# Performance work log

Hardware: AMD Instinct MI355X
Metric: run time of the kernel (lower is better)

The kernel has to match this reference:

```python
import jax, jax.numpy as jnp
import numpy as np

B, L, D, DC, DH, H, DE, DO, DT = 4, 2048, 256, 256, 32, 8, 1024, 256, 256


def _ln(x, g, b, eps=1e-5):
    m = jnp.mean(x, -1, keepdims=True)
    v = jnp.mean((x - m) ** 2, -1, keepdims=True)
    return (x - m) * jax.lax.rsqrt(v + eps) * g + b


def setup_inputs() -> dict:
    key = jax.random.key(0)
    ks = jax.random.split(key, 16)

    def p(k, shape, s=0.02):
        return jax.random.normal(k, shape, jnp.float32) * s

    return dict(
        x=jax.random.normal(ks[0], (B, L, D), jnp.float32),
        context=jax.random.normal(ks[1], (B, L, DC), jnp.float32),
        t=jax.random.normal(ks[2], (B, DT), jnp.float32),
        pos_enc=jax.random.normal(ks[3], (1, L, D), jnp.float32),
        ln_g=jnp.ones(D), ln_b=jnp.zeros(D),
        Wq=p(ks[4], (D, DH * H)), bq=jnp.zeros(DH * H),
        Wkv1=p(ks[5], (DC, DC)), bkv1=jnp.zeros(DC),
        kvln_g=jnp.ones(DC), kvln_b=jnp.zeros(DC),
        Wkv2=p(ks[6], (DC, (DH + D) * H)), bkv2=jnp.zeros((DH + D) * H),
        Wm=p(ks[7], (D * H, D)), bm=jnp.zeros(D),
        Wt1=p(ks[8], (DT, DT)), bt1=jnp.zeros(DT),
        Wt2=p(ks[9], (DT, D + DE)), bt2=jnp.zeros(D + DE),
        ff1ln_g=jnp.ones(D), ff1ln_b=jnp.zeros(D),
        Wff1=p(ks[10], (D, DE)), bff1=jnp.zeros(DE),
        Wff2=p(ks[11], (DE, DO)), bff2=jnp.zeros(DO),
    )


def reference(x, context, t, pos_enc, ln_g, ln_b, Wq, bq, Wkv1, bkv1,
              kvln_g, kvln_b, Wkv2, bkv2, Wm, bm, Wt1, bt1, Wt2, bt2,
              ff1ln_g, ff1ln_b, Wff1, bff1, Wff2, bff2):
    silu = jax.nn.silu
    # q_proj = Swish -> Linear, applied to ln(x) + pos_enc
    q = silu(_ln(x, ln_g, ln_b) + pos_enc) @ Wq + bq          # [B,L,H*DH]
    q = q.reshape(B, L, H, DH)
    # kv_proj = Linear -> LayerNorm -> Swish -> Linear
    kv = silu(_ln(context @ Wkv1 + bkv1, kvln_g, kvln_b)) @ Wkv2 + bkv2
    k = kv[..., : DH * H].reshape(B, L, H, DH)
    v = kv[..., DH * H:].reshape(B, L, H, D)                   # v head dim = d_in
    scale = DH ** -0.5
    attn = jnp.einsum('bnhc,bmhc->bhnm', q, k) * scale         # [B,H,L,L]
    # mask = 1 - triu(ones): True strictly BELOW the diagonal (anti-causal)
    mask = jnp.tril(jnp.ones((L, L), bool), -1)
    attn = jnp.where(mask, -jnp.inf, attn)
    attn = jax.nn.softmax(attn, axis=-1)
    out = jnp.einsum('bhnm,bmhc->bnhc', attn, v).reshape(B, L, H * D)
    x = x + out @ Wm + bm
    # FiLM time conditioning: [B, d_in+d_expand] -> [B, 1, ...]
    th = silu(t @ Wt1 + bt1) @ Wt2 + bt2
    t_shift = th[:, None, :D]
    t_scale = th[:, None, D:]
    h = silu(_ln(x + t_shift, ff1ln_g, ff1ln_b)) @ Wff1 + bff1
    # ff2 = Swish -> Dropout(eval) -> Linear; shortcut is Identity (d_in == d_out)
    return silu(h * jax.nn.sigmoid(t_scale)) @ Wff2 + bff2 + x
```

## Files before the change

kernel.cpp:

```cpp
#include <hip/hip_runtime.h>
#include <hip/hip_bf16.h>

#define DEVI __device__ __forceinline__
using u16 = unsigned short;
using u32 = unsigned int;

typedef __attribute__((ext_vector_type(4))) float f32x4;
typedef __attribute__((ext_vector_type(8))) __bf16 bf16x8;

constexpr int L_ = 2048;

DEVI u16 f2bf(float f){
  u32 u = __builtin_bit_cast(u32, f);
  u32 r = u + 0x7FFFu + ((u >> 16) & 1u);
  return (u16)(r >> 16);
}
DEVI float sigm(float x){ return 1.f / (1.f + __expf(-x)); }

DEVI f32x4 mfma16(bf16x8 a, bf16x8 b, f32x4 c){
  return __builtin_amdgcn_mfma_f32_16x16x32_bf16(a, b, c, 0, 0, 0);
}

DEVI void gload16(const u16* src, u16* lds){
  __builtin_amdgcn_global_load_lds(
      (const __attribute__((address_space(1))) u32*)src,
      (__attribute__((address_space(3))) u32*)lds, 16, 0, 0);
}
DEVI void gload4(const u16* src, u16* lds){
  __builtin_amdgcn_global_load_lds(
      (const __attribute__((address_space(1))) u32*)src,
      (__attribute__((address_space(3))) u32*)lds, 4, 0, 0);
}

#define WAITV(N) asm volatile("s_waitcnt vmcnt(" #N ")" ::: "memory")

__global__ __launch_bounds__(256)
void prep_all(const float* __restrict__ Wq,   u16* __restrict__ wtq,
              const float* __restrict__ Wkv1, u16* __restrict__ wtkv1,
              const float* __restrict__ Wkv2, u16* __restrict__ wtkv2,
              const float* __restrict__ Wm,   u16* __restrict__ wtm,
              const float* __restrict__ Wff1, u16* __restrict__ wtff1,
              const float* __restrict__ Wff2, u16* __restrict__ wtff2,
              const float* __restrict__ tvec, const float* __restrict__ Wt1,
              const float* __restrict__ bt1,  float* __restrict__ ub,
              const float* __restrict__ ctx,  u16* __restrict__ ctx_bf,
              const float* __restrict__ x,    const float* __restrict__ pos,
              const float* __restrict__ ln_g, const float* __restrict__ ln_b,
              u16* __restrict__ qin_bf){
  __shared__ float smem[32 * 33];
  const int id = blockIdx.x;
  if (id >= 3780){
    const int row  = (id - 3780) * 4 + (threadIdx.x >> 6);
    const int lane = threadIdx.x & 63;
    const long base = (long)row * 256 + lane * 4;
    float4 x4 = *(const float4*)(x + base);
    float v[4] = {x4.x, x4.y, x4.z, x4.w};
    float s = v[0] + v[1] + v[2] + v[3];
    #pragma unroll
    for (int d = 1; d < 64; d <<= 1) s += __shfl_xor(s, d);
    const float mean = s * (1.f / 256.f);
    float q = 0.f;
    #pragma unroll
    for (int i = 0; i < 4; ++i){ float dd = v[i] - mean; q += dd * dd; }
    #pragma unroll
    for (int d = 1; d < 64; d <<= 1) q += __shfl_xor(q, d);
    const float rstd = rsqrtf(q * (1.f / 256.f) + 1e-5f);
    float4 g4 = *(const float4*)(ln_g + lane * 4);
    float4 b4 = *(const float4*)(ln_b + lane * 4);
    float4 pp = *(const float4*)(pos + (long)(row & (L_ - 1)) * 256 + lane * 4);
    float gv[4] = {g4.x, g4.y, g4.z, g4.w}, bb[4] = {b4.x, b4.y, b4.z, b4.w};
    float pe[4] = {pp.x, pp.y, pp.z, pp.w};
    ushort4 o; u16 tmp[4];
    #pragma unroll
    for (int i = 0; i < 4; ++i){
      float y = (v[i] - mean) * rstd * gv[i] + bb[i] + pe[i];
      y = y * sigm(y);
      tmp[i] = f2bf(y);
    }
    o.x = tmp[0]; o.y = tmp[1]; o.z = tmp[2]; o.w = tmp[3];
    *(ushort4*)(qin_bf + base) = o;
    return;
  }
  if (id >= 1732){
    long i = ((long)(id - 1732) * 256 + threadIdx.x) * 4;
    float4 v = *(const float4*)(ctx + i);
    ushort4 o; o.x = f2bf(v.x); o.y = f2bf(v.y); o.z = f2bf(v.z); o.w = f2bf(v.w);
    *(ushort4*)(ctx_bf + i) = o;
    return;
  }
  if (id >= 1728){
    int b = id - 1728, j = threadIdx.x;
    smem[j] = tvec[b * 256 + j];
    __syncthreads();
    float acc = bt1[j];
    for (int k = 0; k < 256; ++k) acc += smem[k] * Wt1[k * 256 + j];
    ub[b * 256 + j] = acc * sigm(acc);
    return;
  }
  const float* W; u16* WT; int K, N, local, nx;
  if      (id <   64){ W = Wq;   WT = wtq;   K = 256;  N = 256;  local = id;        nx = 8;  }
  else if (id <  128){ W = Wkv1; WT = wtkv1; K = 256;  N = 256;  local = id - 64;   nx = 8;  }
  else if (id <  704){ W = Wkv2; WT = wtkv2; K = 256;  N = 2304; local = id - 128;  nx = 72; }
  else if (id < 1216){ W = Wm;   WT = wtm;   K = 2048; N = 256;  local = id - 704;  nx = 8;  }
  else if (id < 1472){ W = Wff1; WT = wtff1; K = 256;  N = 1024; local = id - 1216; nx = 32; }
  else               { W = Wff2; WT = wtff2; K = 1024; N = 256;  local = id - 1472; nx = 8;  }
  int n0 = (local % nx) * 32, k0 = (local / nx) * 32;
  float (*tile)[33] = (float(*)[33])smem;
  int tx = threadIdx.x & 31, ty = threadIdx.x >> 5;
  #pragma unroll
  for (int i = 0; i < 4; ++i){ int kk = ty + i*8; tile[kk][tx] = W[(long)(k0+kk)*N + n0 + tx]; }
  __syncthreads();
  #pragma unroll
  for (int i = 0; i < 4; ++i){ int nn = ty + i*8; WT[(long)(n0+nn)*K + k0 + tx] = f2bf(tile[tx][nn]); }
}

template<int MODE>
__global__ __launch_bounds__(256)
void ln_silu(const float* __restrict__ in, const float* __restrict__ add,
             const float* __restrict__ g, const float* __restrict__ bvec,
             u16* __restrict__ out){
  const int row  = blockIdx.x * 4 + (threadIdx.x >> 6);
  const int lane = threadIdx.x & 63;
  const long base = (long)row * 256 + lane * 4;
  float4 x4 = *(const float4*)(in + base);
  float v[4] = {x4.x, x4.y, x4.z, x4.w};
  if constexpr (MODE == 2){
    float4 s4 = *(const float4*)(add + (row >> 11) * 1280 + lane * 4);
    v[0] += s4.x; v[1] += s4.y; v[2] += s4.z; v[3] += s4.w;
  }
  float s = v[0] + v[1] + v[2] + v[3];
  #pragma unroll
  for (int d = 1; d < 64; d <<= 1) s += __shfl_xor(s, d);
  const float mean = s * (1.f / 256.f);
  float q = 0.f;
  #pragma unroll
  for (int i = 0; i < 4; ++i){ float dd = v[i] - mean; q += dd * dd; }
  #pragma unroll
  for (int d = 1; d < 64; d <<= 1) q += __shfl_xor(q, d);
  const float rstd = rsqrtf(q * (1.f / 256.f) + 1e-5f);
  float4 g4 = *(const float4*)(g + lane * 4);
  float4 b4 = *(const float4*)(bvec + lane * 4);
  float gv[4] = {g4.x, g4.y, g4.z, g4.w}, bb[4] = {b4.x, b4.y, b4.z, b4.w};
  ushort4 o; u16 tmp[4];
  #pragma unroll
  for (int i = 0; i < 4; ++i){
    float y = (v[i] - mean) * rstd * gv[i] + bb[i];
    y = y * sigm(y);
    tmp[i] = f2bf(y);
  }
  o.x = tmp[0]; o.y = tmp[1]; o.z = tmp[2]; o.w = tmp[3];
  *(ushort4*)(out + base) = o;
}

template<int EPI>
DEVI void gemm_body(const u16* __restrict__ A, const u16* __restrict__ BT,
                    const float* __restrict__ bias, const float* __restrict__ res,
                    const float* __restrict__ thv,
                    float* __restrict__ outF, u16* __restrict__ outB, u16* __restrict__ outB2,
                    int N, int K, u16* smem, int by){
  u16* As = smem;
  u16* Bs = smem + 3 * 4096;
  const int t = threadIdx.x, lane = t & 63;
  const int lr = lane & 15, lg = lane >> 4;
  const int wv = t >> 6;
  const int wrow = (wv >> 2) * 32;
  const int wcol = (wv & 3) * 32;
  const long bm = (long)blockIdx.x * 64, bn = (long)by * 128;

  auto stage = [&](int step, int buf){
    const int kt = step * 64;
    {
      int o = t * 16;
      int row = o >> 7, cb = o & 127;
      int scb = cb ^ ((row & 7) << 4);
      gload16(&A[(bm + row) * K + kt + (scb >> 1)], &As[buf * 4096 + (o >> 1)]);
    }
    #pragma unroll
    for (int i = 0; i < 2; ++i){
      int o = t * 16 + i * 8192;
      int row = o >> 7, cb = o & 127;
      int scb = cb ^ ((row & 7) << 4);
      gload16(&BT[(bn + row) * K + kt + (scb >> 1)], &Bs[buf * 8192 + (o >> 1)]);
    }
  };

  const f32x4 zero = {0.f, 0.f, 0.f, 0.f};
  f32x4 acc[2][2];
  acc[0][0] = zero; acc[0][1] = zero; acc[1][0] = zero; acc[1][1] = zero;

  const int ns = K >> 6;
  stage(0, 0); stage(1, 1);
  int bufc = 0;
  for (int i = 0; i < ns; ++i){
    if (i + 1 < ns) WAITV(3); else WAITV(0);
    __builtin_amdgcn_s_barrier();
    __builtin_amdgcn_sched_barrier(0);
    if (i + 2 < ns){
      int nb = bufc + 2; if (nb >= 3) nb -= 3;
      stage(i + 2, nb);
    }
    __builtin_amdgcn_s_setprio(1);
    #pragma unroll
    for (int ks = 0; ks < 2; ++ks){
      bf16x8 av[2], bv[2];
      const int cb = (ks * 32 + lg * 8) * 2;
      #pragma unroll
      for (int m = 0; m < 2; ++m){
        int row = wrow + m * 16 + lr;
        av[m] = *(const bf16x8*)((const char*)&As[bufc * 4096] + row * 128 + (cb ^ ((row & 7) << 4)));
      }
      #pragma unroll
      for (int n = 0; n < 2; ++n){
        int row = wcol + n * 16 + lr;
        bv[n] = *(const bf16x8*)((const char*)&Bs[bufc * 8192] + row * 128 + (cb ^ ((row & 7) << 4)));
      }
      #pragma unroll
      for (int m = 0; m < 2; ++m)
        #pragma unroll
        for (int n = 0; n < 2; ++n)
          acc[m][n] = mfma16(av[m], bv[n], acc[m][n]);
    }
    __builtin_amdgcn_s_setprio(0);
    bufc = (bufc + 1 == 3) ? 0 : bufc + 1;
  }

  constexpr float QSC = 0.17677669529663687f * 1.4426950408889634f;

  if constexpr (EPI == 3){
    if (by >= 2){
      __syncthreads();
      u16* tile = smem;
      #pragma unroll
      for (int m = 0; m < 2; ++m)
        #pragma unroll
        for (int n = 0; n < 2; ++n){
          int c_l = wcol + n * 16 + lr;
          long col = bn + c_l;
          int rbase = wrow + m * 16 + lg * 4;
          ushort4 pk;
          u16* pp = (u16*)&pk;
          #pragma unroll
          for (int r = 0; r < 4; ++r)
            pp[r] = f2bf(acc[m][n][r] + bias[col]);
          *(ushort4*)&tile[c_l * 72 + rbase] = pk;
        }
      __syncthreads();
      const int b = (int)(bm >> 11), l0 = (int)(bm & 2047);
      const int hdb = (int)bn - 256;
      const int h = hdb >> 8, d0 = hdb & 255;
      const int dd = t >> 2, lh = (t & 3) * 16;
      u16* dst = outB2 + ((long)((b * 8 + h) * 256 + d0 + dd)) * 2048 + l0 + lh;
      *(uint4*)(dst + 0) = *(const uint4*)&tile[dd * 72 + lh + 0];
      *(uint4*)(dst + 8) = *(const uint4*)&tile[dd * 72 + lh + 8];
      return;
    }
    #pragma unroll
    for (int m = 0; m < 2; ++m)
      #pragma unroll
      for (int n = 0; n < 2; ++n)
        #pragma unroll
        for (int r = 0; r < 4; ++r){
          long row = bm + wrow + m * 16 + lg * 4 + r;
          long col = bn + wcol + n * 16 + lr;
          outB[row * 256 + col] = f2bf(acc[m][n][r] + bias[col]);
        }
    return;
  }

  #pragma unroll
  for (int m = 0; m < 2; ++m)
    #pragma unroll
    for (int n = 0; n < 2; ++n)
      #pragma unroll
      for (int r = 0; r < 4; ++r){
        long row = bm + wrow + m * 16 + lg * 4 + r;
        long col = bn + wcol + n * 16 + lr;
        float v = acc[m][n][r] + bias[col];
        if constexpr (EPI == 0){
          outB[row * N + col] = f2bf(v);
        } else if constexpr (EPI == 1){
          outF[row * N + col] = v;
        } else if constexpr (EPI == 2){
          outF[row * N + col] = v + res[row * N + col];
        } else if constexpr (EPI == 4){
          int b = (int)(row >> 11);
          float ts = thv[b * 1280 + 256 + (int)col];
          float z = v * sigm(ts);
          outB[row * N + col] = f2bf(z * sigm(z));
        } else {
          outB[row * N + col] = f2bf(v * QSC);
        }
      }
}

template<int EPI>
__global__ __launch_bounds__(512, 4)
void gemm2(const u16* __restrict__ A, const u16* __restrict__ BT,
           const float* __restrict__ bias, const float* __restrict__ res,
           const float* __restrict__ thv,
           float* __restrict__ outF, u16* __restrict__ outB, u16* __restrict__ outB2,
           int M, int N, int K){
  __shared__ u16 smem[3 * 4096 + 3 * 8192];
  gemm_body<EPI>(A, BT, bias, res, thv, outF, outB, outB2, N, K, smem, blockIdx.y);
}

template<int E0, int E1>
__global__ __launch_bounds__(512, 4)
void gemm2_dual(const u16* __restrict__ A0, const u16* __restrict__ B0,
                const float* __restrict__ bias0, u16* __restrict__ out0,
                const u16* __restrict__ A1, const u16* __restrict__ B1,
                const float* __restrict__ bias1, float* __restrict__ out1,
                const float* __restrict__ ub, const float* __restrict__ Wt2,
                const float* __restrict__ bt2, float* __restrict__ th,
                int N, int K){
  __shared__ u16 smem[3 * 4096 + 3 * 8192];
  if (blockIdx.y == 4){
    if (blockIdx.x >= 20) return;
    float* us = (float*)smem;
    int local = blockIdx.x, b = local & 3, jb = local >> 2;
    int tj = threadIdx.x & 255;
    us[tj] = ub[b * 256 + tj];
    __syncthreads();
    int j = jb * 256 + tj;
    float acc = bt2[j];
    for (int k = 0; k < 256; ++k) acc += us[k] * Wt2[k * 1280 + j];
    th[b * 1280 + j] = acc;
    return;
  }
  if (blockIdx.y < 2)
    gemm_body<E0>(A0, B0, bias0, nullptr, nullptr, nullptr, out0, nullptr, N, K, smem, blockIdx.y);
  else
    gemm_body<E1>(A1, B1, bias1, nullptr, nullptr, out1, nullptr, nullptr, N, K, smem, blockIdx.y - 2);
}

__global__ __launch_bounds__(256, 2)
void gemm3(const u16* __restrict__ A, const u16* __restrict__ BT,
           const float* __restrict__ bias, const float* __restrict__ res,
           float* __restrict__ outF, int M, int N, int K){
  __shared__ u16 smem[3 * 2048 + 3 * 8192];
  u16* As = smem;
  u16* Bs = smem + 3 * 2048;
  const int t = threadIdx.x, lane = t & 63;
  const int lr = lane & 15, lg = lane >> 4;
  const int wcol = (t >> 6) * 32;
  const long bm = (long)blockIdx.x * 32, bn = (long)blockIdx.y * 128;

  auto stage = [&](int step, int buf){
    const int kt = step * 64;
    {
      int o = t * 16;
      int row = o >> 7, cb = o & 127;
      int scb = cb ^ ((row & 7) << 4);
      gload16(&A[(bm + row) * K + kt + (scb >> 1)], &As[buf * 2048 + (o >> 1)]);
    }
    #pragma unroll
    for (int i = 0; i < 4; ++i){
      int o = t * 16 + i * 4096;
      int row = o >> 7, cb = o & 127;
      int scb = cb ^ ((row & 7) << 4);
      gload16(&BT[(bn + row) * K + kt + (scb >> 1)], &Bs[buf * 8192 + (o >> 1)]);
    }
  };

  const f32x4 zero = {0.f, 0.f, 0.f, 0.f};
  f32x4 acc[2][2];
  acc[0][0] = zero; acc[0][1] = zero; acc[1][0] = zero; acc[1][1] = zero;

  const int ns = K >> 6;
  stage(0, 0); stage(1, 1);
  int bufc = 0;
  for (int i = 0; i < ns; ++i){
    if (i + 1 < ns) WAITV(5); else WAITV(0);
    __builtin_amdgcn_s_barrier();
    __builtin_amdgcn_sched_barrier(0);
    if (i + 2 < ns){
      int nb = bufc + 2; if (nb >= 3) nb -= 3;
      stage(i + 2, nb);
    }
    __builtin_amdgcn_s_setprio(1);
    #pragma unroll
    for (int ks = 0; ks < 2; ++ks){
      bf16x8 av[2], bv[2];
      const int cb = (ks * 32 + lg * 8) * 2;
      #pragma unroll
      for (int m = 0; m < 2; ++m){
        int row = m * 16 + lr;
        av[m] = *(const bf16x8*)((const char*)&As[bufc * 2048] + row * 128 + (cb ^ ((row & 7) << 4)));
      }
      #pragma unroll
      for (int n = 0; n < 2; ++n){
        int row = wcol + n * 16 + lr;
        bv[n] = *(const bf16x8*)((const char*)&Bs[bufc * 8192] + row * 128 + (cb ^ ((row & 7) << 4)));
      }
      #pragma unroll
      for (int m = 0; m < 2; ++m)
        #pragma unroll
        for (int n = 0; n < 2; ++n)
          acc[m][n] = mfma16(av[m], bv[n], acc[m][n]);
    }
    __builtin_amdgcn_s_setprio(0);
    bufc = (bufc + 1 == 3) ? 0 : bufc + 1;
  }

  #pragma unroll
  for (int m = 0; m < 2; ++m)
    #pragma unroll
    for (int n = 0; n < 2; ++n)
      #pragma unroll
      for (int r = 0; r < 4; ++r){
        long row = bm + m * 16 + lg * 4 + r;
        long col = bn + wcol + n * 16 + lr;
        float v = acc[m][n][r] + bias[col];
        outF[row * N + col] = v + res[row * N + col];
      }
}

__global__ __launch_bounds__(512, 2)
void attn7(const u16* __restrict__ Q, const u16* __restrict__ Kb,
           const u16* __restrict__ VT, u16* __restrict__ attout){
  const int bh = blockIdx.x, b = bh >> 3, h = bh & 7;
  const int p  = blockIdx.y;
  const int t  = threadIdx.x;
  const int w  = t >> 6, lane = t & 63, lr = lane & 15, lg = lane >> 4;

  __shared__ u16 Vs[3][256 * 64];
  __shared__ u16 Ks[3][64 * 32];
  __shared__ u16 Ps[8][16 * 64];
  u16* myP = &Ps[w][0];

  const f32x4 zero = {0.f, 0.f, 0.f, 0.f};
  const u16* vbase = VT + (long)bh * 256 * 2048;
  const u16* kbase = Kb + (long)(b * L_) * 256 + h * 32;

  auto stage = [&](int m0, int buf){
    #pragma unroll
    for (int i = 0; i < 4; ++i){
      int ob = t * 16 + i * 8192;
      int d = ob >> 7, cb = ob & 127;
      int scb = cb ^ ((d & 7) << 4);
      gload16(vbase + (long)d * 2048 + m0 + (scb >> 1), &Vs[buf][ob >> 1]);
    }
    #pragma unroll
    for (int i = 0; i < 2; ++i){
      int g = t + i * 512;
      int row = g >> 4, sl = g & 15;
      int scol = ((sl & 3) << 1) + ((((sl >> 2) ^ (row & 3))) << 3);
      gload4(kbase + (long)(m0 + row) * 256 + scol, &Ks[buf][g << 1]);
    }
  };

  for (int half = 0; half < 2; ++half){
    const int chunk = half ? (15 - p) : p;
    const int n0 = chunk * 128;
    const int n_lo = n0 + w * 16;
    const int nt = (L_ - n0) >> 6;

    bf16x8 qf = *(const bf16x8*)(Q + ((long)(b * L_ + n_lo + lr)) * 256 + h * 32 + lg * 8);

    f32x4 o[16];
    #pragma unroll
    for (int c2 = 0; c2 < 16; ++c2) o[c2] = zero;
    float mrun = -1e30f, srun = 0.f;

    stage(n0, 0); stage(n0 + 64, 1);

    int bufc = 0;
    for (int tt = 0; tt < nt; ++tt){
      const int m0 = n0 + tt * 64;
      if (tt + 1 < nt) WAITV(6); else WAITV(0);
      __builtin_amdgcn_s_barrier();
      __builtin_amdgcn_sched_barrier(0);
      if (tt + 2 < nt){
        int nb = bufc + 2; if (nb >= 3) nb -= 3;
        stage(m0 + 128, nb);
      }

      if (m0 + 64 > n_lo){
        const bool partial = (m0 < n_lo + 16);

        bf16x8 kf[4];
        #pragma unroll
        for (int c = 0; c < 4; ++c){
          int row = c * 16 + lr;
          kf[c] = *(const bf16x8*)&Ks[bufc][row * 32 + ((lg ^ (row & 3)) << 3)];
        }
        f32x4 sc[4];
        #pragma unroll
        for (int c = 0; c < 4; ++c)
          sc[c] = mfma16(kf[c], qf, zero);

        if (partial){
          #pragma unroll
          for (int c = 0; c < 4; ++c)
            #pragma unroll
            for (int r = 0; r < 4; ++r)
              if ((m0 + c * 16 + lg * 4 + r) < (n_lo + lr)) sc[c][r] = -1e30f;
        }

        float t0 = fmaxf(fmaxf(sc[0][0], sc[0][1]), fmaxf(sc[0][2], sc[0][3]));
        #pragma unroll
        for (int c = 1; c < 4; ++c)
          t0 = fmaxf(t0, fmaxf(fmaxf(sc[c][0], sc[c][1]), fmaxf(sc[c][2], sc[c][3])));
        t0 = fmaxf(t0, __shfl_xor(t0, 16));
        t0 = fmaxf(t0, __shfl_xor(t0, 32));
        const bool needl = (t0 > mrun + 11.5f);
        if (__any(needl)){
          float mn  = fmaxf(mrun, t0);
          float frc = exp2f(mrun - mn);
          mrun = mn; srun *= frc;
          float f0 = __shfl(frc, lg * 4 + 0), f1 = __shfl(frc, lg * 4 + 1);
          float f2 = __shfl(frc, lg * 4 + 2), f3 = __shfl(frc, lg * 4 + 3);
          f32x4 fv = {f0, f1, f2, f3};
          #pragma unroll
          for (int c2 = 0; c2 < 16; ++c2) o[c2] *= fv;
        }

        {
          const int q = lr, sw = (q & 7) << 3;
          float rs = 0.f;
          #pragma unroll
          for (int c = 0; c < 4; ++c){
            float e0 = exp2f(sc[c][0] - mrun);
            float e1 = exp2f(sc[c][1] - mrun);
            float e2 = exp2f(sc[c][2] - mrun);
            float e3 = exp2f(sc[c][3] - mrun);
            if (partial && mrun < -1e29f){ e0 = e1 = e2 = e3 = 0.f; }
            rs += (e0 + e1) + (e2 + e3);
            ushort4 pk;
            pk.x = __builtin_bit_cast(u16, (__bf16)e0);
            pk.y = __builtin_bit_cast(u16, (__bf16)e1);
            pk.z = __builtin_bit_cast(u16, (__bf16)e2);
            pk.w = __builtin_bit_cast(u16, (__bf16)e3);
            *(ushort4*)&myP[q * 64 + ((c * 16 + lg * 4) ^ sw)] = pk;
          }
          rs += __shfl_xor(rs, 16);
          rs += __shfl_xor(rs, 32);
          srun += rs;
        }

        __builtin_amdgcn_s_setprio(1);
        #pragma unroll
        for (int ks = 0; ks < 2; ++ks){
          bf16x8 pa = *(const bf16x8*)&myP[lr * 64 + ((ks * 32 + lg * 8) ^ ((lr & 7) << 3))];
          #pragma unroll
          for (int c2 = 0; c2 < 16; ++c2){
            const int d = c2 * 16 + lr;
            bf16x8 vf = *(const bf16x8*)((const char*)&Vs[bufc][0] + d * 128 +
                                         ((ks * 64 + lg * 16) ^ ((d & 7) << 4)));
            o[c2] = mfma16(pa, vf, o[c2]);
          }
        }
        __builtin_amdgcn_s_setprio(0);
      }
      bufc = (bufc + 1 == 3) ? 0 : bufc + 1;
    }

    {
      float invc = 1.f / srun;
      #pragma unroll
      for (int r = 0; r < 4; ++r){
        float inv = __shfl(invc, lg * 4 + r);
        long row = (long)(b * L_ + n_lo + lg * 4 + r);
        #pragma unroll
        for (int c2 = 0; c2 < 16; ++c2)
          attout[row * 2048 + h * 256 + c2 * 16 + lr] = f2bf(o[c2][r] * inv);
      }
    }
    WAITV(0);
    __syncthreads();
  }
}

extern "C" void kernel_launch(void* const* d_in, const int* in_sizes, int n_in,
                              void* d_out, int out_size, void* d_ws, size_t ws_size,
                              hipStream_t stream){
  (void)in_sizes; (void)n_in; (void)out_size; (void)ws_size;
  const float* x    = (const float*)d_in[0];
  const float* ctx  = (const float*)d_in[1];
  const float* tin  = (const float*)d_in[2];
  const float* pos  = (const float*)d_in[3];
  const float* ln_g = (const float*)d_in[4];
  const float* ln_b = (const float*)d_in[5];
  const float* Wq   = (const float*)d_in[6];
  const float* bq   = (const float*)d_in[7];
  const float* Wkv1 = (const float*)d_in[8];
  const float* bkv1 = (const float*)d_in[9];
  const float* kvg  = (const float*)d_in[10];
  const float* kvb  = (const float*)d_in[11];
  const float* Wkv2 = (const float*)d_in[12];
  const float* bkv2 = (const float*)d_in[13];
  const float* Wm   = (const float*)d_in[14];
  const float* bm   = (const float*)d_in[15];
  const float* Wt1  = (const float*)d_in[16];
  const float* bt1  = (const float*)d_in[17];
  const float* Wt2  = (const float*)d_in[18];
  const float* bt2  = (const float*)d_in[19];
  const float* fg   = (const float*)d_in[20];
  const float* fb   = (const float*)d_in[21];
  const float* Wff1 = (const float*)d_in[22];
  const float* bff1 = (const float*)d_in[23];
  const float* Wff2 = (const float*)d_in[24];
  const float* bff2 = (const float*)d_in[25];

  char* ws = (char*)d_ws;
  u16*   wt_q   = (u16*)  (ws + 0);
  u16*   wt_kv1 = (u16*)  (ws + 131072);
  u16*   wt_kv2 = (u16*)  (ws + 262144);
  u16*   wt_m   = (u16*)  (ws + 1441792);
  u16*   wt_ff1 = (u16*)  (ws + 2490368);
  u16*   wt_ff2 = (u16*)  (ws + 3014656);
  u16*   ctx_bf = (u16*)  (ws + 3538944);
  u16*   qin_bf = (u16*)  (ws + 7733248);
  u16*   q_bf   = (u16*)  (ws + 11927552);
  float* kv1    = (float*)(ws + 16121856);
  u16*   k_bf   = (u16*)  (ws + 24510464);
  u16*   v_bf   = (u16*)  (ws + 28704768);
  u16*   vT     = (u16*)  (ws + 62259200);
  float* ub     = (float*)(ws + 95813632);
  float* th     = (float*)(ws + 95817728);

  prep_all<<<5828, 256, 0, stream>>>(Wq, wt_q, Wkv1, wt_kv1, Wkv2, wt_kv2,
                                     Wm, wt_m, Wff1, wt_ff1, Wff2, wt_ff2,
                                     tin, Wt1, bt1, ub,
                                     ctx, ctx_bf, x, pos, ln_g, ln_b, qin_bf);
  gemm2_dual<5,1><<<dim3(128, 5), 512, 0, stream>>>(qin_bf, wt_q, bq, q_bf,
                                                    ctx_bf, wt_kv1, bkv1, kv1,
                                                    ub, Wt2, bt2, th,
                                                    256, 256);
  ln_silu<1><<<2048, 256, 0, stream>>>(kv1, nullptr, kvg, kvb, qin_bf);
  gemm2<3><<<dim3(128, 18), 512, 0, stream>>>(qin_bf, wt_kv2, bkv2, nullptr, nullptr,
                                              nullptr, k_bf, vT, 8192, 2304, 256);
  attn7<<<dim3(32, 8), 512, 0, stream>>>(q_bf, k_bf, vT, v_bf);
  gemm3<<<dim3(256, 2), 256, 0, stream>>>(v_bf, wt_m, bm, x, kv1, 8192, 256, 2048);
  ln_silu<2><<<2048, 256, 0, stream>>>(kv1, th, fg, fb, ctx_bf);
  gemm2<4><<<dim3(128, 8), 512, 0, stream>>>(ctx_bf, wt_ff1, bff1, nullptr, th,
                                             nullptr, (u16*)vT, nullptr, 8192, 1024, 256);
  gemm3<<<dim3(256, 2), 256, 0, stream>>>((u16*)vT, wt_ff2, bff2, kv1,
                                          (float*)d_out, 8192, 256, 1024);
}
```

Measured before the change: 183.5 us.

## Restructure attention: 4 waves with 32 query rows each, K in registers

The attention kernel moves from 8 waves of 16 query rows, each block handling two paired chunks, to 4 waves of 32 query rows, with one chunk per block over a grid twice as large. Each V fragment read from shared memory now feeds two MFMAs, which halves LDS traffic per unit of compute. K tiles are loaded straight into registers with a prefetch one step ahead instead of being staged through LDS, and V triple buffering becomes double buffering. In exchange it doubles the output accumulator registers, which may raise spilling or lower occupancy, and loses some load-balance pairing within a block.

```diff
diff --git a/kernel.cpp b/kernel.cpp
--- a/kernel.cpp
+++ b/kernel.cpp
@@ -25,11 +25,6 @@
   __builtin_amdgcn_global_load_lds(
       (const __attribute__((address_space(1))) u32*)src,
       (__attribute__((address_space(3))) u32*)lds, 16, 0, 0);
-}
-DEVI void gload4(const u16* src, u16* lds){
-  __builtin_amdgcn_global_load_lds(
-      (const __attribute__((address_space(1))) u32*)src,
-      (__attribute__((address_space(3))) u32*)lds, 4, 0, 0);
 }
 
 #define WAITV(N) asm volatile("s_waitcnt vmcnt(" #N ")" ::: "memory")
@@ -415,159 +410,178 @@
       }
 }
 
-__global__ __launch_bounds__(512, 2)
-void attn7(const u16* __restrict__ Q, const u16* __restrict__ Kb,
-           const u16* __restrict__ VT, u16* __restrict__ attout){
+__global__ __launch_bounds__(256, 2)
+void attn11(const u16* __restrict__ Q, const u16* __restrict__ Kb,
+            const u16* __restrict__ VT, u16* __restrict__ attout){
   const int bh = blockIdx.x, b = bh >> 3, h = bh & 7;
-  const int p  = blockIdx.y;
-  const int t  = threadIdx.x;
-  const int w  = t >> 6, lane = t & 63, lr = lane & 15, lg = lane >> 4;
-
-  __shared__ u16 Vs[3][256 * 64];
-  __shared__ u16 Ks[3][64 * 32];
-  __shared__ u16 Ps[8][16 * 64];
+  const int yc = blockIdx.y;
+  const int chunk = (yc < 8) ? yc : 23 - yc;
+  const int n0 = chunk * 128;
+  const int t = threadIdx.x;
+  const int w = t >> 6, lane = t & 63, lr = lane & 15, lg = lane >> 4;
+  const int n_lo = n0 + w * 32;
+  const int nt = (L_ - n0) >> 6;
+
+  __shared__ u16 Vs[2][256 * 64];
+  __shared__ u16 Ps[4][32 * 64];
   u16* myP = &Ps[w][0];
 
   const f32x4 zero = {0.f, 0.f, 0.f, 0.f};
   const u16* vbase = VT + (long)bh * 256 * 2048;
   const u16* kbase = Kb + (long)(b * L_) * 256 + h * 32;
 
-  auto stage = [&](int m0, int buf){
-    #pragma unroll
-    for (int i = 0; i < 4; ++i){
-      int ob = t * 16 + i * 8192;
+  auto stageV = [&](int m0, int buf){
+    #pragma unroll
+    for (int i = 0; i < 8; ++i){
+      int ob = t * 16 + i * 4096;
       int d = ob >> 7, cb = ob & 127;
       int scb = cb ^ ((d & 7) << 4);
       gload16(vbase + (long)d * 2048 + m0 + (scb >> 1), &Vs[buf][ob >> 1]);
     }
-    #pragma unroll
-    for (int i = 0; i < 2; ++i){
-      int g = t + i * 512;
-      int row = g >> 4, sl = g & 15;
-      int scol = ((sl & 3) << 1) + ((((sl >> 2) ^ (row & 3))) << 3);
-      gload4(kbase + (long)(m0 + row) * 256 + scol, &Ks[buf][g << 1]);
-    }
   };
 
-  for (int half = 0; half < 2; ++half){
-    const int chunk = half ? (15 - p) : p;
-    const int n0 = chunk * 128;
-    const int n_lo = n0 + w * 16;
-    const int nt = (L_ - n0) >> 6;
-
-    bf16x8 qf = *(const bf16x8*)(Q + ((long)(b * L_ + n_lo + lr)) * 256 + h * 32 + lg * 8);
-
-    f32x4 o[16];
-    #pragma unroll
-    for (int c2 = 0; c2 < 16; ++c2) o[c2] = zero;
-    float mrun = -1e30f, srun = 0.f;
-
-    stage(n0, 0); stage(n0 + 64, 1);
-
-    int bufc = 0;
-    for (int tt = 0; tt < nt; ++tt){
-      const int m0 = n0 + tt * 64;
-      if (tt + 1 < nt) WAITV(6); else WAITV(0);
-      __builtin_amdgcn_s_barrier();
-      __builtin_amdgcn_sched_barrier(0);
-      if (tt + 2 < nt){
-        int nb = bufc + 2; if (nb >= 3) nb -= 3;
-        stage(m0 + 128, nb);
-      }
-
-      if (m0 + 64 > n_lo){
-        const bool partial = (m0 < n_lo + 16);
-
-        bf16x8 kf[4];
-        #pragma unroll
-        for (int c = 0; c < 4; ++c){
-          int row = c * 16 + lr;
-          kf[c] = *(const bf16x8*)&Ks[bufc][row * 32 + ((lg ^ (row & 3)) << 3)];
-        }
-        f32x4 sc[4];
+  bf16x8 qf[2];
+  #pragma unroll
+  for (int qh = 0; qh < 2; ++qh)
+    qf[qh] = *(const bf16x8*)(Q + ((long)(b * L_ + n_lo + qh * 16 + lr)) * 256 + h * 32 + lg * 8);
+
+  f32x4 o[2][16];
+  #pragma unroll
+  for (int qh = 0; qh < 2; ++qh)
+    #pragma unroll
+    for (int c2 = 0; c2 < 16; ++c2) o[qh][c2] = zero;
+  float mrun[2] = {-1e30f, -1e30f}, srun[2] = {0.f, 0.f};
+
+  stageV(n0, 0);
+  bf16x8 kf[4];
+  #pragma unroll
+  for (int c = 0; c < 4; ++c)
+    kf[c] = *(const bf16x8*)(kbase + (long)(n0 + c * 16 + lr) * 256 + lg * 8);
+
+  for (int tt = 0; tt < nt; ++tt){
+    const int m0 = n0 + tt * 64;
+    const int cur = tt & 1;
+    if (tt + 1 < nt) WAITV(4); else WAITV(0);
+    __builtin_amdgcn_s_barrier();
+    __builtin_amdgcn_sched_barrier(0);
+    bf16x8 kfN[4];
+    if (tt + 1 < nt){
+      stageV(m0 + 64, cur ^ 1);
+      #pragma unroll
+      for (int c = 0; c < 4; ++c)
+        kfN[c] = *(const bf16x8*)(kbase + (long)(m0 + 64 + c * 16 + lr) * 256 + lg * 8);
+    }
+
+    if (m0 + 64 > n_lo){
+      const bool partial = (m0 < n_lo + 32);
+
+      f32x4 sc[2][4];
+      #pragma unroll
+      for (int qh = 0; qh < 2; ++qh)
         #pragma unroll
         for (int c = 0; c < 4; ++c)
-          sc[c] = mfma16(kf[c], qf, zero);
-
-        if (partial){
+          sc[qh][c] = mfma16(kf[c], qf[qh], zero);
+
+      if (partial){
+        #pragma unroll
+        for (int qh = 0; qh < 2; ++qh)
           #pragma unroll
           for (int c = 0; c < 4; ++c)
             #pragma unroll
             for (int r = 0; r < 4; ++r)
-              if ((m0 + c * 16 + lg * 4 + r) < (n_lo + lr)) sc[c][r] = -1e30f;
-        }
-
-        float t0 = fmaxf(fmaxf(sc[0][0], sc[0][1]), fmaxf(sc[0][2], sc[0][3]));
+              if ((m0 + c * 16 + lg * 4 + r) < (n_lo + qh * 16 + lr)) sc[qh][c][r] = -1e30f;
+      }
+
+      float tmax[2]; bool needl = false;
+      #pragma unroll
+      for (int qh = 0; qh < 2; ++qh){
+        float t0 = fmaxf(fmaxf(sc[qh][0][0], sc[qh][0][1]), fmaxf(sc[qh][0][2], sc[qh][0][3]));
         #pragma unroll
         for (int c = 1; c < 4; ++c)
-          t0 = fmaxf(t0, fmaxf(fmaxf(sc[c][0], sc[c][1]), fmaxf(sc[c][2], sc[c][3])));
+          t0 = fmaxf(t0, fmaxf(fmaxf(sc[qh][c][0], sc[qh][c][1]),
+                               fmaxf(sc[qh][c][2], sc[qh][c][3])));
         t0 = fmaxf(t0, __shfl_xor(t0, 16));
         t0 = fmaxf(t0, __shfl_xor(t0, 32));
-        const bool needl = (t0 > mrun + 11.5f);
-        if (__any(needl)){
-          float mn  = fmaxf(mrun, t0);
-          float frc = exp2f(mrun - mn);
-          mrun = mn; srun *= frc;
+        tmax[qh] = t0;
+        needl |= (t0 > mrun[qh] + 11.5f);
+      }
+      if (__any(needl)){
+        #pragma unroll
+        for (int qh = 0; qh < 2; ++qh){
+          float mn  = fmaxf(mrun[qh], tmax[qh]);
+          float frc = exp2f(mrun[qh] - mn);
+          mrun[qh] = mn; srun[qh] *= frc;
           float f0 = __shfl(frc, lg * 4 + 0), f1 = __shfl(frc, lg * 4 + 1);
           float f2 = __shfl(frc, lg * 4 + 2), f3 = __shfl(frc, lg * 4 + 3);
           f32x4 fv = {f0, f1, f2, f3};
           #pragma unroll
-          for (int c2 = 0; c2 < 16; ++c2) o[c2] *= fv;
+          for (int c2 = 0; c2 < 16; ++c2) o[qh][c2] *= fv;
         }
-
-        {
-          const int q = lr, sw = (q & 7) << 3;
-          float rs = 0.f;
+      }
+
+      #pragma unroll
+      for (int qh = 0; qh < 2; ++qh){
+        const int q = qh * 16 + lr;
+        const int sw = (q & 7) << 3;
+        float rs = 0.f;
+        #pragma unroll
+        for (int c = 0; c < 4; ++c){
+          float e0 = exp2f(sc[qh][c][0] - mrun[qh]);
+          float e1 = exp2f(sc[qh][c][1] - mrun[qh]);
+          float e2 = exp2f(sc[qh][c][2] - mrun[qh]);
+          float e3 = exp2f(sc[qh][c][3] - mrun[qh]);
+          if (partial && mrun[qh] < -1e29f){ e0 = e1 = e2 = e3 = 0.f; }
+          rs += (e0 + e1) + (e2 + e3);
+          ushort4 pk;
+          pk.x = __builtin_bit_cast(u16, (__bf16)e0);
+          pk.y = __builtin_bit_cast(u16, (__bf16)e1);
+          pk.z = __builtin_bit_cast(u16, (__bf16)e2);
+          pk.w = __builtin_bit_cast(u16, (__bf16)e3);
+          *(ushort4*)&myP[q * 64 + ((c * 16 + lg * 4) ^ sw)] = pk;
+        }
+        rs += __shfl_xor(rs, 16);
+        rs += __shfl_xor(rs, 32);
+        srun[qh] += rs;
+      }
+
+      __builtin_amdgcn_s_setprio(1);
+      #pragma unroll
+      for (int ks = 0; ks < 2; ++ks){
+        bf16x8 pa[2];
+        #pragma unroll
+        for (int qh = 0; qh < 2; ++qh){
+          const int q = qh * 16 + lr;
+          pa[qh] = *(const bf16x8*)&myP[q * 64 + ((ks * 32 + lg * 8) ^ ((q & 7) << 3))];
+        }
+        #pragma unroll
+        for (int c2 = 0; c2 < 16; ++c2){
+          const int d = c2 * 16 + lr;
+          bf16x8 vf = *(const bf16x8*)((const char*)&Vs[cur][0] + d * 128 +
+                                       ((ks * 64 + lg * 16) ^ ((d & 7) << 4)));
           #pragma unroll
-          for (int c = 0; c < 4; ++c){
-            float e0 = exp2f(sc[c][0] - mrun);
-            float e1 = exp2f(sc[c][1] - mrun);
-            float e2 = exp2f(sc[c][2] - mrun);
-            float e3 = exp2f(sc[c][3] - mrun);
-            if (partial && mrun < -1e29f){ e0 = e1 = e2 = e3 = 0.f; }
-            rs += (e0 + e1) + (e2 + e3);
-            ushort4 pk;
-            pk.x = __builtin_bit_cast(u16, (__bf16)e0);
-            pk.y = __builtin_bit_cast(u16, (__bf16)e1);
-            pk.z = __builtin_bit_cast(u16, (__bf16)e2);
-            pk.w = __builtin_bit_cast(u16, (__bf16)e3);
-            *(ushort4*)&myP[q * 64 + ((c * 16 + lg * 4) ^ sw)] = pk;
-          }
-          rs += __shfl_xor(rs, 16);
-          rs += __shfl_xor(rs, 32);
-          srun += rs;
+          for (int qh = 0; qh < 2; ++qh)
+            o[qh][c2] = mfma16(pa[qh], vf, o[qh][c2]);
         }
-
-        __builtin_amdgcn_s_setprio(1);
-        #pragma unroll
-        for (int ks = 0; ks < 2; ++ks){
-          bf16x8 pa = *(const bf16x8*)&myP[lr * 64 + ((ks * 32 + lg * 8) ^ ((lr & 7) << 3))];
-          #pragma unroll
-          for (int c2 = 0; c2 < 16; ++c2){
-            const int d = c2 * 16 + lr;
-            bf16x8 vf = *(const bf16x8*)((const char*)&Vs[bufc][0] + d * 128 +
-                                         ((ks * 64 + lg * 16) ^ ((d & 7) << 4)));
-            o[c2] = mfma16(pa, vf, o[c2]);
-          }
-        }
-        __builtin_amdgcn_s_setprio(0);
-      }
-      bufc = (bufc + 1 == 3) ? 0 : bufc + 1;
-    }
-
-    {
-      float invc = 1.f / srun;
-      #pragma unroll
-      for (int r = 0; r < 4; ++r){
-        float inv = __shfl(invc, lg * 4 + r);
-        long row = (long)(b * L_ + n_lo + lg * 4 + r);
-        #pragma unroll
-        for (int c2 = 0; c2 < 16; ++c2)
-          attout[row * 2048 + h * 256 + c2 * 16 + lr] = f2bf(o[c2][r] * inv);
-      }
-    }
-    WAITV(0);
-    __syncthreads();
+      }
+      __builtin_amdgcn_s_setprio(0);
+    }
+    if (tt + 1 < nt){
+      #pragma unroll
+      for (int c = 0; c < 4; ++c) kf[c] = kfN[c];
+    }
+  }
+
+  #pragma unroll
+  for (int qh = 0; qh < 2; ++qh){
+    float invc = 1.f / srun[qh];
+    #pragma unroll
+    for (int r = 0; r < 4; ++r){
+      float inv = __shfl(invc, lg * 4 + r);
+      long row = (long)(b * L_ + n_lo + qh * 16 + lg * 4 + r);
+      #pragma unroll
+      for (int c2 = 0; c2 < 16; ++c2)
+        attout[row * 2048 + h * 256 + c2 * 16 + lr] = f2bf(o[qh][c2][r] * inv);
+    }
   }
 }
 
@@ -630,7 +644,7 @@
   ln_silu<1><<<2048, 256, 0, stream>>>(kv1, nullptr, kvg, kvb, qin_bf);
   gemm2<3><<<dim3(128, 18), 512, 0, stream>>>(qin_bf, wt_kv2, bkv2, nullptr, nullptr,
                                               nullptr, k_bf, vT, 8192, 2304, 256);
-  attn7<<<dim3(32, 8), 512, 0, stream>>>(q_bf, k_bf, vT, v_bf);
+  attn11<<<dim3(32, 16), 256, 0, stream>>>(q_bf, k_bf, vT, v_bf);
   gemm3<<<dim3(256, 2), 256, 0, stream>>>(v_bf, wt_m, bm, x, kv1, 8192, 256, 2048);
   ln_silu<2><<<2048, 256, 0, stream>>>(kv1, th, fg, fb, ctx_bf);
   gemm2<4><<<dim3(128, 8), 512, 0, stream>>>(ctx_bf, wt_ff1, bff1, nullptr, th,
```

New measurement: 219.2 us. 19.5% more time.

## Restructure attention pipeline into paired 128-key steps with direct K register loads

Applied to the files above, without the earlier changes.

The attention kernel now stages V tiles in pairs of 64-key buffers, one 128-key step at a time, with double buffering (4 buffers). A barrier and full vmcnt wait happen once per 128 keys instead of once per 64. K is no longer staged through LDS with 4-byte async loads; each wave reads its K fragments straight from global memory into registers. This is meant to cut barrier and wait overhead and drop the small K LDS copies. In exchange, per-wave global K loads are uncoalesced and sit on the critical path, and the full vmcnt(0) wait reduces overlap between loads and compute.

```diff
diff --git a/kernel.cpp b/kernel.cpp
--- a/kernel.cpp
+++ b/kernel.cpp
@@ -25,11 +25,6 @@
   __builtin_amdgcn_global_load_lds(
       (const __attribute__((address_space(1))) u32*)src,
       (__attribute__((address_space(3))) u32*)lds, 16, 0, 0);
-}
-DEVI void gload4(const u16* src, u16* lds){
-  __builtin_amdgcn_global_load_lds(
-      (const __attribute__((address_space(1))) u32*)src,
-      (__attribute__((address_space(3))) u32*)lds, 4, 0, 0);
 }
 
 #define WAITV(N) asm volatile("s_waitcnt vmcnt(" #N ")" ::: "memory")
@@ -416,15 +411,14 @@
 }
 
 __global__ __launch_bounds__(512, 2)
-void attn7(const u16* __restrict__ Q, const u16* __restrict__ Kb,
-           const u16* __restrict__ VT, u16* __restrict__ attout){
+void attn13(const u16* __restrict__ Q, const u16* __restrict__ Kb,
+            const u16* __restrict__ VT, u16* __restrict__ attout){
   const int bh = blockIdx.x, b = bh >> 3, h = bh & 7;
   const int p  = blockIdx.y;
   const int t  = threadIdx.x;
   const int w  = t >> 6, lane = t & 63, lr = lane & 15, lg = lane >> 4;
 
-  __shared__ u16 Vs[3][256 * 64];
-  __shared__ u16 Ks[3][64 * 32];
+  __shared__ u16 Vs[4][256 * 64];
   __shared__ u16 Ps[8][16 * 64];
   u16* myP = &Ps[w][0];
 
@@ -432,7 +426,7 @@
   const u16* vbase = VT + (long)bh * 256 * 2048;
   const u16* kbase = Kb + (long)(b * L_) * 256 + h * 32;
 
-  auto stage = [&](int m0, int buf){
+  auto stageV = [&](int m0, int buf){
     #pragma unroll
     for (int i = 0; i < 4; ++i){
       int ob = t * 16 + i * 8192;
@@ -440,20 +434,13 @@
       int scb = cb ^ ((d & 7) << 4);
       gload16(vbase + (long)d * 2048 + m0 + (scb >> 1), &Vs[buf][ob >> 1]);
     }
-    #pragma unroll
-    for (int i = 0; i < 2; ++i){
-      int g = t + i * 512;
-      int row = g >> 4, sl = g & 15;
-      int scol = ((sl & 3) << 1) + ((((sl >> 2) ^ (row & 3))) << 3);
-      gload4(kbase + (long)(m0 + row) * 256 + scol, &Ks[buf][g << 1]);
-    }
   };
 
   for (int half = 0; half < 2; ++half){
     const int chunk = half ? (15 - p) : p;
     const int n0 = chunk * 128;
     const int n_lo = n0 + w * 16;
-    const int nt = (L_ - n0) >> 6;
+    const int ntp = (L_ - n0) >> 7;
 
     bf16x8 qf = *(const bf16x8*)(Q + ((long)(b * L_ + n_lo + lr)) * 256 + h * 32 + lg * 8);
 
@@ -462,97 +449,99 @@
     for (int c2 = 0; c2 < 16; ++c2) o[c2] = zero;
     float mrun = -1e30f, srun = 0.f;
 
-    stage(n0, 0); stage(n0 + 64, 1);
-
-    int bufc = 0;
-    for (int tt = 0; tt < nt; ++tt){
-      const int m0 = n0 + tt * 64;
-      if (tt + 1 < nt) WAITV(6); else WAITV(0);
+    stageV(n0, 0); stageV(n0 + 64, 1);
+
+    auto tilec = [&](const bf16x8* kf, int m0, int buf){
+      if (m0 + 64 <= n_lo) return;
+      const bool partial = (m0 < n_lo + 16);
+
+      f32x4 sc[4];
+      #pragma unroll
+      for (int c = 0; c < 4; ++c)
+        sc[c] = mfma16(kf[c], qf, zero);
+
+      if (partial){
+        #pragma unroll
+        for (int c = 0; c < 4; ++c)
+          #pragma unroll
+          for (int r = 0; r < 4; ++r)
+            if ((m0 + c * 16 + lg * 4 + r) < (n_lo + lr)) sc[c][r] = -1e30f;
+      }
+
+      float t0 = fmaxf(fmaxf(sc[0][0], sc[0][1]), fmaxf(sc[0][2], sc[0][3]));
+      #pragma unroll
+      for (int c = 1; c < 4; ++c)
+        t0 = fmaxf(t0, fmaxf(fmaxf(sc[c][0], sc[c][1]), fmaxf(sc[c][2], sc[c][3])));
+      t0 = fmaxf(t0, __shfl_xor(t0, 16));
+      t0 = fmaxf(t0, __shfl_xor(t0, 32));
+      const bool needl = (t0 > mrun + 11.5f);
+      if (__any(needl)){
+        float mn  = fmaxf(mrun, t0);
+        float frc = exp2f(mrun - mn);
+        mrun = mn; srun *= frc;
+        float f0 = __shfl(frc, lg * 4 + 0), f1 = __shfl(frc, lg * 4 + 1);
+        float f2 = __shfl(frc, lg * 4 + 2), f3 = __shfl(frc, lg * 4 + 3);
+        f32x4 fv = {f0, f1, f2, f3};
+        #pragma unroll
+        for (int c2 = 0; c2 < 16; ++c2) o[c2] *= fv;
+      }
+
+      {
+        const int q = lr, sw = (q & 7) << 3;
+        float rs = 0.f;
+        #pragma unroll
+        for (int c = 0; c < 4; ++c){
+          float e0 = exp2f(sc[c][0] - mrun);
+          float e1 = exp2f(sc[c][1] - mrun);
+          float e2 = exp2f(sc[c][2] - mrun);
+          float e3 = exp2f(sc[c][3] - mrun);
+          if (partial && mrun < -1e29f){ e0 = e1 = e2 = e3 = 0.f; }
+          rs += (e0 + e1) + (e2 + e3);
+          ushort4 pk;
+          pk.x = __builtin_bit_cast(u16, (__bf16)e0);
+          pk.y = __builtin_bit_cast(u16, (__bf16)e1);
+          pk.z = __builtin_bit_cast(u16, (__bf16)e2);
+          pk.w = __builtin_bit_cast(u16, (__bf16)e3);
+          *(ushort4*)&myP[q * 64 + ((c * 16 + lg * 4) ^ sw)] = pk;
+        }
+        rs += __shfl_xor(rs, 16);
+        rs += __shfl_xor(rs, 32);
+        srun += rs;
+      }
+
+      __builtin_amdgcn_s_setprio(1);
+      #pragma unroll
+      for (int ks = 0; ks < 2; ++ks){
+        bf16x8 pa = *(const bf16x8*)&myP[lr * 64 + ((ks * 32 + lg * 8) ^ ((lr & 7) << 3))];
+        #pragma unroll
+        for (int c2 = 0; c2 < 16; ++c2){
+          const int d = c2 * 16 + lr;
+          bf16x8 vf = *(const bf16x8*)((const char*)&Vs[buf][0] + d * 128 +
+                                       ((ks * 64 + lg * 16) ^ ((d & 7) << 4)));
+          o[c2] = mfma16(pa, vf, o[c2]);
+        }
+      }
+      __builtin_amdgcn_s_setprio(0);
+    };
+
+    for (int tp = 0; tp < ntp; ++tp){
+      const int m00 = n0 + tp * 128;
+      const int bb = (tp & 1) << 1;
+      WAITV(0);
       __builtin_amdgcn_s_barrier();
       __builtin_amdgcn_sched_barrier(0);
-      if (tt + 2 < nt){
-        int nb = bufc + 2; if (nb >= 3) nb -= 3;
-        stage(m0 + 128, nb);
-      }
-
-      if (m0 + 64 > n_lo){
-        const bool partial = (m0 < n_lo + 16);
-
-        bf16x8 kf[4];
-        #pragma unroll
-        for (int c = 0; c < 4; ++c){
-          int row = c * 16 + lr;
-          kf[c] = *(const bf16x8*)&Ks[bufc][row * 32 + ((lg ^ (row & 3)) << 3)];
-        }
-        f32x4 sc[4];
-        #pragma unroll
-        for (int c = 0; c < 4; ++c)
-          sc[c] = mfma16(kf[c], qf, zero);
-
-        if (partial){
-          #pragma unroll
-          for (int c = 0; c < 4; ++c)
-            #pragma unroll
-            for (int r = 0; r < 4; ++r)
-              if ((m0 + c * 16 + lg * 4 + r) < (n_lo + lr)) sc[c][r] = -1e30f;
-        }
-
-        float t0 = fmaxf(fmaxf(sc[0][0], sc[0][1]), fmaxf(sc[0][2], sc[0][3]));
-        #pragma unroll
-        for (int c = 1; c < 4; ++c)
-          t0 = fmaxf(t0, fmaxf(fmaxf(sc[c][0], sc[c][1]), fmaxf(sc[c][2], sc[c][3])));
-        t0 = fmaxf(t0, __shfl_xor(t0, 16));
-        t0 = fmaxf(t0, __shfl_xor(t0, 32));
-        const bool needl = (t0 > mrun + 11.5f);
-        if (__any(needl)){
-          float mn  = fmaxf(mrun, t0);
-          float frc = exp2f(mrun - mn);
-          mrun = mn; srun *= frc;
-          float f0 = __shfl(frc, lg * 4 + 0), f1 = __shfl(frc, lg * 4 + 1);
-          float f2 = __shfl(frc, lg * 4 + 2), f3 = __shfl(frc, lg * 4 + 3);
-          f32x4 fv = {f0, f1, f2, f3};
-          #pragma unroll
-          for (int c2 = 0; c2 < 16; ++c2) o[c2] *= fv;
-        }
-
-        {
-          const int q = lr, sw = (q & 7) << 3;
-          float rs = 0.f;
-          #pragma unroll
-          for (int c = 0; c < 4; ++c){
-            float e0 = exp2f(sc[c][0] - mrun);
-            float e1 = exp2f(sc[c][1] - mrun);
-            float e2 = exp2f(sc[c][2] - mrun);
-            float e3 = exp2f(sc[c][3] - mrun);
-            if (partial && mrun < -1e29f){ e0 = e1 = e2 = e3 = 0.f; }
-            rs += (e0 + e1) + (e2 + e3);
-            ushort4 pk;
-            pk.x = __builtin_bit_cast(u16, (__bf16)e0);
-            pk.y = __builtin_bit_cast(u16, (__bf16)e1);
-            pk.z = __builtin_bit_cast(u16, (__bf16)e2);
-            pk.w = __builtin_bit_cast(u16, (__bf16)e3);
-            *(ushort4*)&myP[q * 64 + ((c * 16 + lg * 4) ^ sw)] = pk;
-          }
-          rs += __shfl_xor(rs, 16);
-          rs += __shfl_xor(rs, 32);
-          srun += rs;
-        }
-
-        __builtin_amdgcn_s_setprio(1);
-        #pragma unroll
-        for (int ks = 0; ks < 2; ++ks){
-          bf16x8 pa = *(const bf16x8*)&myP[lr * 64 + ((ks * 32 + lg * 8) ^ ((lr & 7) << 3))];
-          #pragma unroll
-          for (int c2 = 0; c2 < 16; ++c2){
-            const int d = c2 * 16 + lr;
-            bf16x8 vf = *(const bf16x8*)((const char*)&Vs[bufc][0] + d * 128 +
-                                         ((ks * 64 + lg * 16) ^ ((d & 7) << 4)));
-            o[c2] = mfma16(pa, vf, o[c2]);
-          }
-        }
-        __builtin_amdgcn_s_setprio(0);
-      }
-      bufc = (bufc + 1 == 3) ? 0 : bufc + 1;
+      if (tp + 1 < ntp){
+        stageV(m00 + 128, bb ^ 2);
+        stageV(m00 + 192, (bb ^ 2) + 1);
+      }
+      bf16x8 kf0[4], kf1[4];
+      #pragma unroll
+      for (int c = 0; c < 4; ++c){
+        kf0[c] = *(const bf16x8*)(kbase + (long)(m00 + c * 16 + lr) * 256 + lg * 8);
+        kf1[c] = *(const bf16x8*)(kbase + (long)(m00 + 64 + c * 16 + lr) * 256 + lg * 8);
+      }
+      tilec(kf0, m00,      bb);
+      tilec(kf1, m00 + 64, bb + 1);
     }
 
     {
@@ -630,7 +619,7 @@
   ln_silu<1><<<2048, 256, 0, stream>>>(kv1, nullptr, kvg, kvb, qin_bf);
   gemm2<3><<<dim3(128, 18), 512, 0, stream>>>(qin_bf, wt_kv2, bkv2, nullptr, nullptr,
                                               nullptr, k_bf, vT, 8192, 2304, 256);
-  attn7<<<dim3(32, 8), 512, 0, stream>>>(q_bf, k_bf, vT, v_bf);
+  attn13<<<dim3(32, 8), 512, 0, stream>>>(q_bf, k_bf, vT, v_bf);
   gemm3<<<dim3(256, 2), 256, 0, stream>>>(v_bf, wt_m, bm, x, kv1, 8192, 256, 2048);
   ln_silu<2><<<2048, 256, 0, stream>>>(kv1, th, fg, fb, ctx_bf);
   gemm2<4><<<dim3(128, 8), 512, 0, stream>>>(ctx_bf, wt_ff1, bff1, nullptr, th,
```

Measured after the change: 202.4 us. +10.3%, slower.
